# Optimization experiments

Hardware: AMD Instinct MI355X
Metric: run time of the kernel (lower is better)

## Reference

```python
import jax, jax.numpy as jnp
import numpy as np

LOW_T = 0.05
HIGH_T = 0.15

SOBEL_X = jnp.array([[-1., 0., 1.], [-2., 0., 2.], [-1., 0., 1.]], dtype=jnp.float32).reshape(1, 1, 3, 3)
SOBEL_Y = jnp.array([[1., 2., 1.], [0., 0., 0.], [-1., -2., -1.]], dtype=jnp.float32).reshape(1, 1, 3, 3)


def _conv3x3(x, k):
    # NCHW conv, padding=1, stride=1 (matches F.conv2d(x, k, padding=1))
    return jax.lax.conv_general_dilated(x, k, window_strides=(1, 1), padding=((1, 1), (1, 1)))


def setup_inputs() -> dict:
    key = jax.random.key(0)
    x = jax.random.normal(key, (1, 1, 4096, 4096), dtype=jnp.float32)
    return {"x": x}


def reference(x):
    grad_x = _conv3x3(x, SOBEL_X)
    grad_y = _conv3x3(x, SOBEL_Y)
    grad_mag = jnp.sqrt(grad_x * grad_x + grad_y * grad_y)
    grad_dir = jnp.arctan2(grad_y, grad_x)  # radians, as in the original (compared to degree thresholds)

    m = grad_mag[0, 0]  # [H, W]
    d = grad_dir[0, 0][1:-1, 1:-1]  # direction at interior pixels [H-2, W-2]
    H, W = m.shape

    def sh(dr, dc):
        # magnitude at (row+dr, col+dc) for interior pixels
        return m[1 + dr:H - 1 + dr, 1 + dc:W - 1 + dc]

    mc = sh(0, 0)

    # Branch predicates replicated literally from the torch code (degree thresholds
    # vs radian values; some sub-conditions are vacuously false, kept for faithfulness).
    b1 = ((d >= -22.5) & (d <= 22.5)) | ((d >= 157.5) & (d <= 180.0)) | ((d >= -157.5) & (d <= -180.0))
    b2 = ((d > 22.5) & (d <= 67.5)) | ((d >= -112.5) & (d < -157.5))
    b3 = ((d > 67.5) & (d <= 112.5)) | ((d >= -67.5) & (d < -22.5))

    mag_prev = jnp.where(b1, sh(0, -1), jnp.where(b2, sh(-1, 1), jnp.where(b3, sh(-1, 0), sh(-1, -1))))
    mag_next = jnp.where(b1, sh(0, 1), jnp.where(b2, sh(1, -1), jnp.where(b3, sh(1, 0), sh(1, 1))))

    keep = (mc >= mag_prev) & (mc >= mag_next)
    interior = jnp.where(keep, mc, jnp.zeros_like(mc))
    edges = jnp.zeros_like(m).at[1:-1, 1:-1].set(interior)

    # Double thresholding: strong -> 255, weak ([low, high]) -> 0, below-low passes through.
    strong = edges > HIGH_T
    weak = (edges >= LOW_T) & (edges <= HIGH_T)
    out = jnp.where(strong, jnp.float32(255.0), jnp.where(weak, jnp.float32(0.0), edges))
    return out  # [H, W]
```

## Files before the change

### kernel.cpp

```cpp
#include <hip/hip_runtime.h>
#include <math.h>


constexpr int Wd = 4096;
constexpr int Ht = 4096;

typedef float f4 __attribute__((ext_vector_type(4)));

__global__ __launch_bounds__(256) void canny_kernel(const float* __restrict__ x,
                                                    float* __restrict__ out) {
    const int tid  = threadIdx.x;
    const int lane = tid & 63;
    const int r    = blockIdx.y * 4 + (tid >> 6);
    const int wc   = blockIdx.x;
    const int cbase = wc * 256;
    const int c     = cbase + lane * 4;

    const int rm = r > 0 ? r - 1 : 0;
    const int rp = r < Ht - 1 ? r + 1 : Ht - 1;

    const float* rowa = x + (size_t)rm * Wd;
    const float* rowb = x + (size_t)r  * Wd;
    const float* rowc = x + (size_t)rp * Wd;

    f4 a  = *(const f4*)(rowa + c);
    f4 b  = *(const f4*)(rowb + c);
    f4 cc = *(const f4*)(rowc + c);

    float t1[4], t2[4];
    #pragma unroll
    for (int j = 0; j < 4; ++j) {
        t1[j] = a[j] + 2.0f * b[j] + cc[j];
        t2[j] = a[j] - cc[j];
    }

    float hl1[2] = {0.f, 0.f}, hl2[2] = {0.f, 0.f};
    float hr1[2] = {0.f, 0.f}, hr2[2] = {0.f, 0.f};
    if (lane == 0 && wc > 0) {
        f4 ha = *(const f4*)(rowa + cbase - 4);
        f4 hb = *(const f4*)(rowb + cbase - 4);
        f4 hc = *(const f4*)(rowc + cbase - 4);
        hl1[0] = ha[2] + 2.0f * hb[2] + hc[2];  hl2[0] = ha[2] - hc[2];
        hl1[1] = ha[3] + 2.0f * hb[3] + hc[3];  hl2[1] = ha[3] - hc[3];
    }
    if (lane == 63 && wc < 15) {
        f4 ha = *(const f4*)(rowa + cbase + 256);
        f4 hb = *(const f4*)(rowb + cbase + 256);
        f4 hc = *(const f4*)(rowc + cbase + 256);
        hr1[0] = ha[0] + 2.0f * hb[0] + hc[0];  hr2[0] = ha[0] - hc[0];
        hr1[1] = ha[1] + 2.0f * hb[1] + hc[1];  hr2[1] = ha[1] - hc[1];
    }

    float l1a = __shfl_up(t1[2], 1),  l1b = __shfl_up(t1[3], 1);
    float l2a = __shfl_up(t2[2], 1),  l2b = __shfl_up(t2[3], 1);
    float r1a = __shfl_down(t1[0], 1), r1b = __shfl_down(t1[1], 1);
    float r2a = __shfl_down(t2[0], 1), r2b = __shfl_down(t2[1], 1);
    if (lane == 0)  { l1a = hl1[0]; l1b = hl1[1]; l2a = hl2[0]; l2b = hl2[1]; }
    if (lane == 63) { r1a = hr1[0]; r1b = hr1[1]; r2a = hr2[0]; r2b = hr2[1]; }

    float T1[8] = {l1a, l1b, t1[0], t1[1], t1[2], t1[3], r1a, r1b};
    float T2[8] = {l2a, l2b, t2[0], t2[1], t2[2], t2[3], r2a, r2b};

    float q[6];
    #pragma unroll
    for (int i = 0; i < 6; ++i) {
        float gx = T1[i + 2] - T1[i];
        float gy = T2[i] + 2.0f * T2[i + 1] + T2[i + 2];
        q[i] = gx * gx + gy * gy;
    }

    const float C1  = __uint_as_float(0x3CB851EDu);
    const float C2B = __uint_as_float(0x3B23D709u);

    bool hazard = false;
    #pragma unroll
    for (int i = 0; i < 5; ++i) {
        int d = (int)(__float_as_uint(q[i + 1]) - __float_as_uint(q[i]));
        hazard |= ((unsigned)(d + 8) < 17u);
    }

    float acc[4];
    #pragma unroll
    for (int o = 0; o < 4; ++o) {
        float qp = q[o], qc = q[o + 1], qn = q[o + 2];
        bool keep = (qc >= qp) && (qc >= qn);
        acc[o] = (keep && qc > C1) ? 255.0f : 0.0f;
        hazard |= (keep && qc > 0.0f && qc <= C2B);
    }

    if (__any(hazard)) {
        float m[6];
        #pragma unroll
        for (int i = 0; i < 6; ++i) m[i] = sqrtf(q[i]);
        #pragma unroll
        for (int o = 0; o < 4; ++o) {
            float mc = m[o + 1];
            bool keep = (mc >= m[o]) && (mc >= m[o + 2]);
            float e = keep ? mc : 0.0f;
            acc[o] = (e > 0.15f) ? 255.0f : ((e >= 0.05f) ? 0.0f : e);
        }
    }

    if (r == 0 || r == Ht - 1) {
        #pragma unroll
        for (int o = 0; o < 4; ++o) acc[o] = 0.0f;
    }
    if (wc == 0  && lane == 0)  acc[0] = 0.0f;
    if (wc == 15 && lane == 63) acc[3] = 0.0f;

    f4 v = {acc[0], acc[1], acc[2], acc[3]};
    *(f4*)(out + (size_t)r * Wd + c) = v;
}

extern "C" void kernel_launch(void* const* d_in, const int* in_sizes, int n_in,
                              void* d_out, int out_size, void* d_ws, size_t ws_size,
                              hipStream_t stream) {
    const float* x = (const float*)d_in[0];
    float* out = (float*)d_out;
    dim3 grid(16, 1024);
    canny_kernel<<<grid, dim3(256), 0, stream>>>(x, out);
}
```

Measured before the change: 117.7 us.

## Process eight rows per wave with register sliding window and nontemporal stores

Each wavefront now computes eight consecutive output rows. It loads ten input rows into registers once, instead of reloading three rows for every output row, so global and L2 read traffic drops from about three reads per row to about 1.25. Halo columns are loaded as 2-float vectors per row. Output stores are switched to nontemporal. The grid shrinks eightfold, which means fewer waves to hide latency and higher register pressure.

```diff
diff --git a/kernel.cpp b/kernel.cpp
--- a/kernel.cpp
+++ b/kernel.cpp
@@ -4,112 +4,118 @@
 
 constexpr int Wd = 4096;
 constexpr int Ht = 4096;
+constexpr int ROWS = 8;
 
 typedef float f4 __attribute__((ext_vector_type(4)));
+typedef float f2 __attribute__((ext_vector_type(2)));
 
 __global__ __launch_bounds__(256) void canny_kernel(const float* __restrict__ x,
                                                     float* __restrict__ out) {
     const int tid  = threadIdx.x;
     const int lane = tid & 63;
-    const int r    = blockIdx.y * 4 + (tid >> 6);
+    const int wv   = tid >> 6;
     const int wc   = blockIdx.x;
     const int cbase = wc * 256;
     const int c     = cbase + lane * 4;
+    const int r0    = (blockIdx.y * 4 + wv) * ROWS;
 
-    const int rm = r > 0 ? r - 1 : 0;
-    const int rp = r < Ht - 1 ? r + 1 : Ht - 1;
+    const bool needL = (lane == 0)  && (wc > 0);
+    const bool needR = (lane == 63) && (wc < 15);
+    const f2 z2 = {0.f, 0.f};
 
-    const float* rowa = x + (size_t)rm * Wd;
-    const float* rowb = x + (size_t)r  * Wd;
-    const float* rowc = x + (size_t)rp * Wd;
-
-    f4 a  = *(const f4*)(rowa + c);
-    f4 b  = *(const f4*)(rowb + c);
-    f4 cc = *(const f4*)(rowc + c);
-
-    float t1[4], t2[4];
+    f4 X[ROWS + 2];
+    f2 HL[ROWS + 2], HR[ROWS + 2];
     #pragma unroll
-    for (int j = 0; j < 4; ++j) {
-        t1[j] = a[j] + 2.0f * b[j] + cc[j];
-        t2[j] = a[j] - cc[j];
-    }
-
-    float hl1[2] = {0.f, 0.f}, hl2[2] = {0.f, 0.f};
-    float hr1[2] = {0.f, 0.f}, hr2[2] = {0.f, 0.f};
-    if (lane == 0 && wc > 0) {
-        f4 ha = *(const f4*)(rowa + cbase - 4);
-        f4 hb = *(const f4*)(rowb + cbase - 4);
-        f4 hc = *(const f4*)(rowc + cbase - 4);
-        hl1[0] = ha[2] + 2.0f * hb[2] + hc[2];  hl2[0] = ha[2] - hc[2];
-        hl1[1] = ha[3] + 2.0f * hb[3] + hc[3];  hl2[1] = ha[3] - hc[3];
-    }
-    if (lane == 63 && wc < 15) {
-        f4 ha = *(const f4*)(rowa + cbase + 256);
-        f4 hb = *(const f4*)(rowb + cbase + 256);
-        f4 hc = *(const f4*)(rowc + cbase + 256);
-        hr1[0] = ha[0] + 2.0f * hb[0] + hc[0];  hr2[0] = ha[0] - hc[0];
-        hr1[1] = ha[1] + 2.0f * hb[1] + hc[1];  hr2[1] = ha[1] - hc[1];
-    }
-
-    float l1a = __shfl_up(t1[2], 1),  l1b = __shfl_up(t1[3], 1);
-    float l2a = __shfl_up(t2[2], 1),  l2b = __shfl_up(t2[3], 1);
-    float r1a = __shfl_down(t1[0], 1), r1b = __shfl_down(t1[1], 1);
-    float r2a = __shfl_down(t2[0], 1), r2b = __shfl_down(t2[1], 1);
-    if (lane == 0)  { l1a = hl1[0]; l1b = hl1[1]; l2a = hl2[0]; l2b = hl2[1]; }
-    if (lane == 63) { r1a = hr1[0]; r1b = hr1[1]; r2a = hr2[0]; r2b = hr2[1]; }
-
-    float T1[8] = {l1a, l1b, t1[0], t1[1], t1[2], t1[3], r1a, r1b};
-    float T2[8] = {l2a, l2b, t2[0], t2[1], t2[2], t2[3], r2a, r2b};
-
-    float q[6];
-    #pragma unroll
-    for (int i = 0; i < 6; ++i) {
-        float gx = T1[i + 2] - T1[i];
-        float gy = T2[i] + 2.0f * T2[i + 1] + T2[i + 2];
-        q[i] = gx * gx + gy * gy;
+    for (int k = 0; k < ROWS + 2; ++k) {
+        int rr = r0 - 1 + k;
+        rr = rr < 0 ? 0 : (rr > Ht - 1 ? Ht - 1 : rr);
+        const float* row = x + (size_t)rr * Wd;
+        X[k]  = *(const f4*)(row + c);
+        HL[k] = needL ? *(const f2*)(row + cbase - 2)   : z2;
+        HR[k] = needR ? *(const f2*)(row + cbase + 256) : z2;
     }
 
     const float C1  = __uint_as_float(0x3CB851EDu);
     const float C2B = __uint_as_float(0x3B23D709u);
 
-    bool hazard = false;
     #pragma unroll
-    for (int i = 0; i < 5; ++i) {
-        int d = (int)(__float_as_uint(q[i + 1]) - __float_as_uint(q[i]));
-        hazard |= ((unsigned)(d + 8) < 17u);
+    for (int o = 0; o < ROWS; ++o) {
+        const int r = r0 + o;
+        f4 a = X[o], b = X[o + 1], cc = X[o + 2];
+
+        float t1[4], t2[4];
+        #pragma unroll
+        for (int j = 0; j < 4; ++j) {
+            t1[j] = a[j] + 2.0f * b[j] + cc[j];
+            t2[j] = a[j] - cc[j];
+        }
+
+        float L1x = HL[o].x + 2.0f * HL[o + 1].x + HL[o + 2].x;
+        float L1y = HL[o].y + 2.0f * HL[o + 1].y + HL[o + 2].y;
+        float L2x = HL[o].x - HL[o + 2].x;
+        float L2y = HL[o].y - HL[o + 2].y;
+        float R1x = HR[o].x + 2.0f * HR[o + 1].x + HR[o + 2].x;
+        float R1y = HR[o].y + 2.0f * HR[o + 1].y + HR[o + 2].y;
+        float R2x = HR[o].x - HR[o + 2].x;
+        float R2y = HR[o].y - HR[o + 2].y;
+
+        float l1a = __shfl_up(t1[2], 1),   l1b = __shfl_up(t1[3], 1);
+        float l2a = __shfl_up(t2[2], 1),   l2b = __shfl_up(t2[3], 1);
+        float r1a = __shfl_down(t1[0], 1), r1b = __shfl_down(t1[1], 1);
+        float r2a = __shfl_down(t2[0], 1), r2b = __shfl_down(t2[1], 1);
+        if (lane == 0)  { l1a = L1x; l1b = L1y; l2a = L2x; l2b = L2y; }
+        if (lane == 63) { r1a = R1x; r1b = R1y; r2a = R2x; r2b = R2y; }
+
+        float T1[8] = {l1a, l1b, t1[0], t1[1], t1[2], t1[3], r1a, r1b};
+        float T2[8] = {l2a, l2b, t2[0], t2[1], t2[2], t2[3], r2a, r2b};
+
+        float q[6];
+        #pragma unroll
+        for (int i = 0; i < 6; ++i) {
+            float gx = T1[i + 2] - T1[i];
+            float gy = T2[i] + 2.0f * T2[i + 1] + T2[i + 2];
+            q[i] = gx * gx + gy * gy;
+        }
+
+        bool hazard = false;
+        #pragma unroll
+        for (int i = 0; i < 5; ++i) {
+            int d = (int)(__float_as_uint(q[i + 1]) - __float_as_uint(q[i]));
+            hazard |= ((unsigned)(d + 8) < 17u);
+        }
+
+        float acc[4];
+        #pragma unroll
+        for (int o2 = 0; o2 < 4; ++o2) {
+            float qp = q[o2], qc = q[o2 + 1], qn = q[o2 + 2];
+            bool keep = (qc >= qp) && (qc >= qn);
+            acc[o2] = (keep && qc > C1) ? 255.0f : 0.0f;
+            hazard |= (keep && qc > 0.0f && qc <= C2B);
+        }
+
+        if (__any(hazard)) {
+            float m[6];
+            #pragma unroll
+            for (int i = 0; i < 6; ++i) m[i] = sqrtf(q[i]);
+            #pragma unroll
+            for (int o2 = 0; o2 < 4; ++o2) {
+                float mc = m[o2 + 1];
+                bool keep = (mc >= m[o2]) && (mc >= m[o2 + 2]);
+                float e = keep ? mc : 0.0f;
+                acc[o2] = (e > 0.15f) ? 255.0f : ((e >= 0.05f) ? 0.0f : e);
+            }
+        }
+
+        if (r == 0 || r == Ht - 1) {
+            #pragma unroll
+            for (int o2 = 0; o2 < 4; ++o2) acc[o2] = 0.0f;
+        }
+        if (wc == 0  && lane == 0)  acc[0] = 0.0f;
+        if (wc == 15 && lane == 63) acc[3] = 0.0f;
+
+        f4 v = {acc[0], acc[1], acc[2], acc[3]};
+        __builtin_nontemporal_store(v, (f4*)(out + (size_t)r * Wd + c));
     }
-
-    float acc[4];
-    #pragma unroll
-    for (int o = 0; o < 4; ++o) {
-        float qp = q[o], qc = q[o + 1], qn = q[o + 2];
-        bool keep = (qc >= qp) && (qc >= qn);
-        acc[o] = (keep && qc > C1) ? 255.0f : 0.0f;
-        hazard |= (keep && qc > 0.0f && qc <= C2B);
-    }
-
-    if (__any(hazard)) {
-        float m[6];
-        #pragma unroll
-        for (int i = 0; i < 6; ++i) m[i] = sqrtf(q[i]);
-        #pragma unroll
-        for (int o = 0; o < 4; ++o) {
-            float mc = m[o + 1];
-            bool keep = (mc >= m[o]) && (mc >= m[o + 2]);
-            float e = keep ? mc : 0.0f;
-            acc[o] = (e > 0.15f) ? 255.0f : ((e >= 0.05f) ? 0.0f : e);
-        }
-    }
-
-    if (r == 0 || r == Ht - 1) {
-        #pragma unroll
-        for (int o = 0; o < 4; ++o) acc[o] = 0.0f;
-    }
-    if (wc == 0  && lane == 0)  acc[0] = 0.0f;
-    if (wc == 15 && lane == 63) acc[3] = 0.0f;
-
-    f4 v = {acc[0], acc[1], acc[2], acc[3]};
-    *(f4*)(out + (size_t)r * Wd + c) = v;
 }
 
 extern "C" void kernel_launch(void* const* d_in, const int* in_sizes, int n_in,
@@ -117,6 +123,6 @@
                               hipStream_t stream) {
     const float* x = (const float*)d_in[0];
     float* out = (float*)d_out;
-    dim3 grid(16, 1024);
+    dim3 grid(16, 128);
     canny_kernel<<<grid, dim3(256), 0, stream>>>(x, out);
 }
```

Measured after the change: 113.3 us. -3.8%, faster.
